# Optimization experiments

Measured on AMD Instinct MI355X. Metric: run time of the kernel, lower is better.

## Reference

```python
import jax, jax.numpy as jnp
import numpy as np

# SMPL kinematic tree: parent index of each of the 24 joints (root's parent unused)
PARENTS = (0, 0, 0, 0, 1, 2, 3, 4, 5, 6, 7, 8, 9, 9, 9, 12, 13, 14, 16, 17, 18, 19, 20, 21)
NUM_JOINTS = 24
BATCH = 131072


def setup_inputs() -> dict:
    key = jax.random.key(0)
    k1, k2 = jax.random.split(key)
    joint_rotations = jax.random.normal(k1, (BATCH, NUM_JOINTS, 3, 3), dtype=jnp.float32)
    joint_positions = jax.random.normal(k2, (BATCH, NUM_JOINTS, 3), dtype=jnp.float32)
    return {"joint_rotations": joint_rotations, "joint_positions": joint_positions}


def reference(joint_rotations, joint_positions):
    B = joint_rotations.shape[0]
    J = NUM_JOINTS
    pos = joint_positions[..., None]  # [B, J, 3, 1]

    # Relative (bone-local) translations: root keeps absolute position.
    parents_arr = jnp.asarray(PARENTS, dtype=jnp.int32)
    rel = pos - pos[:, parents_arr]            # [B, J, 3, 1]; rel[:,0] == 0
    rel = rel.at[:, 0].set(pos[:, 0])          # root uses absolute position

    # Build all local affine transforms at once: [B, J, 4, 4]
    rot_homo = jnp.pad(joint_rotations, ((0, 0), (0, 0), (0, 1), (0, 0)))  # [B,J,4,3]
    trans_homo = jnp.concatenate([rel, jnp.ones((B, J, 1, 1), rel.dtype)], axis=2)  # [B,J,4,1]
    local = jnp.concatenate([rot_homo, trans_homo], axis=3)  # [B,J,4,4]

    # Sequential parent-to-child chain over the static tree (23 tiny batched matmuls).
    transforms = [local[:, 0]]
    for j in range(1, J):
        transforms.append(jnp.matmul(transforms[PARENTS[j]], local[:, j]))
    transforms = jnp.stack(transforms, axis=1)  # [B, J, 4, 4]

    joint_positions_posed = transforms[:, :, :3, 3]  # [B, J, 3]

    # Subtract the transform applied to the rest pose (standard SMPL trick).
    zeros = jnp.zeros((B, J, 1, 1), pos.dtype)
    joint_rest = jnp.concatenate([pos, zeros], axis=2)   # [B, J, 4, 1]
    init_bone = jnp.matmul(transforms, joint_rest)       # [B, J, 4, 1]
    init_bone = jnp.pad(init_bone, ((0, 0), (0, 0), (0, 0), (3, 0)))  # [B, J, 4, 4]
    joint_transforms = transforms - init_bone
    return (joint_transforms, joint_positions_posed)
```

## Files before the change

### kernel.cpp

```cpp
#include <hip/hip_runtime.h>

namespace {
constexpr int NB  = 131072;
constexpr int NJ  = 24;
constexpr int PAR[NJ] = {0,0,0,0,1,2,3,4,5,6,7,8,9,9,9,12,13,14,16,17,18,19,20,21};
constexpr int BLK = 64;
constexpr int BPB = 16;
constexpr int QS  = 17;
constexpr int PSF = 28;
constexpr int LDSF4 = BPB * QS;
}

typedef float f32x4 __attribute__((ext_vector_type(4)));

__global__ __launch_bounds__(BLK) void pose_kernel(
    const float* __restrict__ rot,
    const float* __restrict__ pos,
    float* __restrict__ outT,
    float* __restrict__ outP)
{
    __shared__ __align__(16) f32x4 lds[LDSF4];
    float* ldsf = reinterpret_cast<float*>(lds);

    const int t  = threadIdx.x;
    const int r  = t & 3;
    const int bl = t >> 2;
    const int b0 = blockIdx.x * BPB;
    const int b  = b0 + bl;

    const float* prow = pos + (size_t)b * 72;
    const float* rrow = rot + (size_t)b * 216;

    const bool r0 = (r == 0), r1 = (r == 1), r2 = (r == 2);

    float rows[NJ][3];
    float tg[NJ];
    float carry1[9];
    float carry2[6];
    float Pg[24];

    #pragma unroll
    for (int g = 0; g < 3; ++g) {
        #pragma unroll
        for (int i = 0; i < 6; ++i) {
            f32x4 v = *reinterpret_cast<const f32x4*>(prow + 24 * g + 4 * i);
            Pg[4*i+0] = v.x; Pg[4*i+1] = v.y; Pg[4*i+2] = v.z; Pg[4*i+3] = v.w;
        }

        #pragma unroll
        for (int q = 0; q < 2; ++q) {
            float buf[36];
            #pragma unroll
            for (int i = 0; i < 9; ++i) {
                f32x4 v = *reinterpret_cast<const f32x4*>(rrow + 72 * g + 36 * q + 4 * i);
                buf[4*i+0] = v.x; buf[4*i+1] = v.y; buf[4*i+2] = v.z; buf[4*i+3] = v.w;
            }

            #pragma unroll
            for (int l = 0; l < 4; ++l) {
                const int j  = 8 * g + 4 * q + l;
                const int pj = PAR[j];
                const float* L = buf + 9 * l;
                const int lj = 3 * j - 24 * g;

                if (j == 0) {
                    #pragma unroll
                    for (int k = 0; k < 3; ++k)
                        rows[0][k] = r0 ? L[k] : r1 ? L[3+k] : r2 ? L[6+k] : 0.0f;
                    tg[0] = r0 ? Pg[0] : r1 ? Pg[1] : r2 ? Pg[2] : 1.0f;
                } else {
                    float pxp, pyp, pzp;
                    if (pj >= 8 * g) {
                        const int lp = 3 * pj - 24 * g;
                        pxp = Pg[lp]; pyp = Pg[lp+1]; pzp = Pg[lp+2];
                    } else if (g == 1) {
                        const int ci = 3 * (pj - 5);
                        pxp = carry1[ci]; pyp = carry1[ci+1]; pzp = carry1[ci+2];
                    } else {
                        const int ci = 3 * (pj - 13);
                        pxp = carry2[ci]; pyp = carry2[ci+1]; pzp = carry2[ci+2];
                    }
                    const float relx = Pg[lj]   - pxp;
                    const float rely = Pg[lj+1] - pyp;
                    const float relz = Pg[lj+2] - pzp;
                    #pragma unroll
                    for (int c = 0; c < 3; ++c) {
                        rows[j][c] = rows[pj][0] * L[c]
                                   + rows[pj][1] * L[3+c]
                                   + rows[pj][2] * L[6+c];
                    }
                    tg[j] = rows[pj][0] * relx + rows[pj][1] * rely
                          + rows[pj][2] * relz + tg[pj];
                }

                const float px = Pg[lj], py = Pg[lj+1], pz = Pg[lj+2];
                const float ib = rows[j][0]*px + rows[j][1]*py + rows[j][2]*pz;
                lds[bl * QS + l * 4 + r] =
                    f32x4{rows[j][0], rows[j][1], rows[j][2], tg[j] - ib};
            }

            {
                float* gp = outT + (size_t)b0 * 384 + (8 * g + 4 * q) * 16;
                #pragma unroll
                for (int i = 0; i < 4; ++i) {
                    int f = t + BLK * i;
                    int br = f >> 4, col = f & 15;
                    f32x4 v = lds[br * QS + col];
                    __builtin_nontemporal_store(
                        v, reinterpret_cast<f32x4*>(gp + (size_t)br * 384 + col * 4));
                }
            }
        }

        if (r < 3) {
            #pragma unroll
            for (int jl = 0; jl < 8; ++jl)
                ldsf[bl * PSF + jl * 3 + r] = tg[8 * g + jl];
        }
        {
            float* gp = outP + (size_t)b0 * 72 + g * 24;
            #pragma unroll
            for (int i = 0; i < 2; ++i) {
                int f = t + BLK * i;
                if (f < BPB * 6) {
                    int br = f / 6, col = f % 6;
                    f32x4 v = *reinterpret_cast<const f32x4*>(&ldsf[br * PSF + col * 4]);
                    __builtin_nontemporal_store(
                        v, reinterpret_cast<f32x4*>(gp + (size_t)br * 72 + col * 4));
                }
            }
        }

        if (g == 0) {
            #pragma unroll
            for (int k = 0; k < 9; ++k) carry1[k] = Pg[15 + k];
        } else if (g == 1) {
            #pragma unroll
            for (int k = 0; k < 6; ++k) carry2[k] = Pg[15 + k];
        }
    }
}

extern "C" void kernel_launch(void* const* d_in, const int* in_sizes, int n_in,
                              void* d_out, int out_size, void* d_ws, size_t ws_size,
                              hipStream_t stream) {
    const float* rot = (const float*)d_in[0];
    const float* pos = (const float*)d_in[1];
    float* outT = (float*)d_out;
    float* outP = outT + (size_t)NB * NJ * 16;
    dim3 grid(NB / BPB), block(BLK);
    hipLaunchKernelGGL(pose_kernel, grid, block, 0, stream, rot, pos, outT, outP);
}
```

Baseline: 77.77 us.

## Assign two transform rows per thread to halve redundant loads per batch

Each thread now computes two rows of the 4x4 global transforms instead of one, so two threads rather than four share a batch element. A 64-thread block therefore covers 32 batch elements instead of 16. The change targets the redundant global loads of rotations and positions that every thread of a batch performed, cutting that duplicated load traffic in half. In exchange each thread holds twice as many accumulator registers, and launch bounds now request a minimum occupancy that may force spilling.

```diff
diff --git a/kernel.cpp b/kernel.cpp
--- a/kernel.cpp
+++ b/kernel.cpp
@@ -5,7 +5,7 @@
 constexpr int NJ  = 24;
 constexpr int PAR[NJ] = {0,0,0,0,1,2,3,4,5,6,7,8,9,9,9,12,13,14,16,17,18,19,20,21};
 constexpr int BLK = 64;
-constexpr int BPB = 16;
+constexpr int BPB = 32;
 constexpr int QS  = 17;
 constexpr int PSF = 28;
 constexpr int LDSF4 = BPB * QS;
@@ -13,7 +13,7 @@
 
 typedef float f32x4 __attribute__((ext_vector_type(4)));
 
-__global__ __launch_bounds__(BLK) void pose_kernel(
+__global__ __launch_bounds__(BLK, 4) void pose_kernel(
     const float* __restrict__ rot,
     const float* __restrict__ pos,
     float* __restrict__ outT,
@@ -23,18 +23,19 @@
     float* ldsf = reinterpret_cast<float*>(lds);
 
     const int t  = threadIdx.x;
-    const int r  = t & 3;
-    const int bl = t >> 2;
+    const int h  = t & 1;
+    const int bl = t >> 1;
     const int b0 = blockIdx.x * BPB;
     const int b  = b0 + bl;
 
     const float* prow = pos + (size_t)b * 72;
     const float* rrow = rot + (size_t)b * 216;
+    const bool h0 = (h == 0);
 
-    const bool r0 = (r == 0), r1 = (r == 1), r2 = (r == 2);
-
-    float rows[NJ][3];
-    float tg[NJ];
+    float rowsA[NJ][3];
+    float rowsB[NJ][3];
+    float tgA[NJ];
+    float tgB[NJ];
     float carry1[9];
     float carry2[6];
     float Pg[24];
@@ -65,9 +66,12 @@
 
                 if (j == 0) {
                     #pragma unroll
-                    for (int k = 0; k < 3; ++k)
-                        rows[0][k] = r0 ? L[k] : r1 ? L[3+k] : r2 ? L[6+k] : 0.0f;
-                    tg[0] = r0 ? Pg[0] : r1 ? Pg[1] : r2 ? Pg[2] : 1.0f;
+                    for (int k = 0; k < 3; ++k) {
+                        rowsA[0][k] = h0 ? L[k]   : L[6+k];
+                        rowsB[0][k] = h0 ? L[3+k] : 0.0f;
+                    }
+                    tgA[0] = h0 ? Pg[0] : Pg[2];
+                    tgB[0] = h0 ? Pg[1] : 1.0f;
                 } else {
                     float pxp, pyp, pzp;
                     if (pj >= 8 * g) {
@@ -85,24 +89,32 @@
                     const float relz = Pg[lj+2] - pzp;
                     #pragma unroll
                     for (int c = 0; c < 3; ++c) {
-                        rows[j][c] = rows[pj][0] * L[c]
-                                   + rows[pj][1] * L[3+c]
-                                   + rows[pj][2] * L[6+c];
+                        rowsA[j][c] = rowsA[pj][0] * L[c]
+                                    + rowsA[pj][1] * L[3+c]
+                                    + rowsA[pj][2] * L[6+c];
+                        rowsB[j][c] = rowsB[pj][0] * L[c]
+                                    + rowsB[pj][1] * L[3+c]
+                                    + rowsB[pj][2] * L[6+c];
                     }
-                    tg[j] = rows[pj][0] * relx + rows[pj][1] * rely
-                          + rows[pj][2] * relz + tg[pj];
+                    tgA[j] = rowsA[pj][0] * relx + rowsA[pj][1] * rely
+                           + rowsA[pj][2] * relz + tgA[pj];
+                    tgB[j] = rowsB[pj][0] * relx + rowsB[pj][1] * rely
+                           + rowsB[pj][2] * relz + tgB[pj];
                 }
 
                 const float px = Pg[lj], py = Pg[lj+1], pz = Pg[lj+2];
-                const float ib = rows[j][0]*px + rows[j][1]*py + rows[j][2]*pz;
-                lds[bl * QS + l * 4 + r] =
-                    f32x4{rows[j][0], rows[j][1], rows[j][2], tg[j] - ib};
+                const float ibA = rowsA[j][0]*px + rowsA[j][1]*py + rowsA[j][2]*pz;
+                const float ibB = rowsB[j][0]*px + rowsB[j][1]*py + rowsB[j][2]*pz;
+                lds[bl * QS + l * 4 + 2 * h + 0] =
+                    f32x4{rowsA[j][0], rowsA[j][1], rowsA[j][2], tgA[j] - ibA};
+                lds[bl * QS + l * 4 + 2 * h + 1] =
+                    f32x4{rowsB[j][0], rowsB[j][1], rowsB[j][2], tgB[j] - ibB};
             }
 
             {
                 float* gp = outT + (size_t)b0 * 384 + (8 * g + 4 * q) * 16;
                 #pragma unroll
-                for (int i = 0; i < 4; ++i) {
+                for (int i = 0; i < 8; ++i) {
                     int f = t + BLK * i;
                     int br = f >> 4, col = f & 15;
                     f32x4 v = lds[br * QS + col];
@@ -112,22 +124,21 @@
             }
         }
 
-        if (r < 3) {
-            #pragma unroll
-            for (int jl = 0; jl < 8; ++jl)
-                ldsf[bl * PSF + jl * 3 + r] = tg[8 * g + jl];
+        #pragma unroll
+        for (int jl = 0; jl < 8; ++jl) {
+            const int j = 8 * g + jl;
+            ldsf[bl * PSF + jl * 3 + 2 * h] = tgA[j];
+            if (h0) ldsf[bl * PSF + jl * 3 + 1] = tgB[j];
         }
         {
             float* gp = outP + (size_t)b0 * 72 + g * 24;
             #pragma unroll
-            for (int i = 0; i < 2; ++i) {
+            for (int i = 0; i < 3; ++i) {
                 int f = t + BLK * i;
-                if (f < BPB * 6) {
-                    int br = f / 6, col = f % 6;
-                    f32x4 v = *reinterpret_cast<const f32x4*>(&ldsf[br * PSF + col * 4]);
-                    __builtin_nontemporal_store(
-                        v, reinterpret_cast<f32x4*>(gp + (size_t)br * 72 + col * 4));
-                }
+                int br = f / 6, col = f % 6;
+                f32x4 v = *reinterpret_cast<const f32x4*>(&ldsf[br * PSF + col * 4]);
+                __builtin_nontemporal_store(
+                    v, reinterpret_cast<f32x4*>(gp + (size_t)br * 72 + col * 4));
             }
         }
 
```

Result: slower. 92.49 us (+18.9%).
